# Kernel tuning notes

Hardware: AMD Instinct MI355X
Metric: run time of the kernel (lower is better)

Reference implementation:

```python
import jax, jax.numpy as jnp
import numpy as np
from jax import lax

D_MODEL = 1024
BATCH = 4
SEQ = 4096
DECAY = 0.9
INPUT_SCALE = 0.1


def setup_inputs() -> dict:
    key = jax.random.key(0)
    k1, k2, k3 = jax.random.split(key, 3)
    scale_in = 1.0 / np.sqrt(D_MODEL)
    return {
        "x": jax.random.normal(k1, (BATCH, SEQ, D_MODEL), dtype=jnp.float32),
        "W_in": jax.random.normal(k2, (D_MODEL, 2 * D_MODEL), dtype=jnp.float32) * scale_in,
        "b_in": jnp.zeros((2 * D_MODEL,), dtype=jnp.float32),
        "W_out": jax.random.normal(k3, (D_MODEL, D_MODEL), dtype=jnp.float32) * scale_in,
        "b_out": jnp.zeros((D_MODEL,), dtype=jnp.float32),
    }


def reference(x, W_in, b_in, W_out, b_out):
    # x: [B, S, D]
    x_proj = jnp.einsum("bsd,de->bse", x, W_in) + b_in  # [B, S, 2D]
    x_gate, x_hidden = jnp.split(x_proj, 2, axis=-1)
    x_gated = jax.nn.sigmoid(x_gate) * jax.nn.silu(x_hidden)  # [B, S, D]

    # gated EMA scan: h_t = 0.9*h_{t-1} + 0.1*g_t, h_0 = 0
    def step(h, g_t):
        h = DECAY * h + INPUT_SCALE * g_t
        return h, h

    g_tm = jnp.swapaxes(x_gated, 0, 1)  # [S, B, D] time-major
    h0 = jnp.zeros((x.shape[0], x.shape[2]), dtype=x.dtype)
    _, hs = lax.scan(step, h0, g_tm)  # [S, B, D]
    hidden_seq = jnp.swapaxes(hs, 0, 1)  # [B, S, D]

    out = jnp.einsum("bsd,de->bse", hidden_seq, W_out) + b_out
    return out
```

## Files before the change

### kernel.cpp

```cpp
#include <hip/hip_runtime.h>
#include <hip/hip_bf16.h>

#define B_   4
#define S_   4096
#define D_   1024
#define M_   (B_ * S_)
#define K_   1024
#define BK   64
#define NT   (K_ / BK)

typedef __attribute__((ext_vector_type(4))) float f32x4;
typedef __attribute__((ext_vector_type(8))) short bf16x8;
typedef unsigned short ushort_t;
typedef unsigned int uint_t;

__device__ inline ushort_t f2bf(float f) {
    union { float f; unsigned u; } v; v.f = f;
    unsigned r = v.u + 0x7fffu + ((v.u >> 16) & 1u);
    return (ushort_t)(r >> 16);
}
__device__ inline float bf2f(ushort_t s) {
    union { unsigned u; float f; } v; v.u = ((unsigned)s) << 16; return v.f;
}

__global__ void convert_x_kernel(const float4* __restrict__ x, ushort_t* __restrict__ xb) {
    int i = blockIdx.x * 256 + threadIdx.x;
    float4 a = x[2 * i], b = x[2 * i + 1];
    union { ushort_t s[8]; uint4 v; } u;
    u.s[0] = f2bf(a.x); u.s[1] = f2bf(a.y); u.s[2] = f2bf(a.z); u.s[3] = f2bf(a.w);
    u.s[4] = f2bf(b.x); u.s[5] = f2bf(b.y); u.s[6] = f2bf(b.z); u.s[7] = f2bf(b.w);
    ((uint4*)xb)[i] = u.v;
}

__global__ void transpose_win_kernel(const float* __restrict__ W, ushort_t* __restrict__ WT) {
    __shared__ float tile[32][33];
    int tx = threadIdx.x, ty = threadIdx.y;
    int n0 = blockIdx.x * 32, k0 = blockIdx.y * 32;
    int ci = (n0 >> 1) + (tx & 15) + ((tx & 16) ? 1024 : 0);
    tile[ty][tx] = W[(long)(k0 + ty) * 2048 + ci];
    __syncthreads();
    WT[(long)(n0 + ty) * 1024 + k0 + tx] = f2bf(tile[tx][ty]);
}

__global__ void transpose_wo_kernel(const float* __restrict__ W, ushort_t* __restrict__ WT) {
    __shared__ float tile[32][33];
    int tx = threadIdx.x, ty = threadIdx.y;
    int n0 = blockIdx.x * 32, k0 = blockIdx.y * 32;
    tile[ty][tx] = W[(long)(k0 + ty) * 1024 + n0 + tx];
    __syncthreads();
    WT[(long)(n0 + ty) * 1024 + k0 + tx] = f2bf(tile[tx][ty]);
}

__device__ inline void stage_half(const char* gtile, char* ldst, int soff0, int soff1, int w) {
    __builtin_amdgcn_global_load_lds((const __attribute__((address_space(1))) void*)(gtile + soff0),
                                     (__attribute__((address_space(3))) void*)(ldst + w * 2048), 16, 0, 0);
    __builtin_amdgcn_global_load_lds((const __attribute__((address_space(1))) void*)(gtile + soff1),
                                     (__attribute__((address_space(3))) void*)(ldst + w * 2048 + 1024), 16, 0, 0);
}

template<int NBN, int GATE>
__global__ __launch_bounds__(512, 2) void gemm8_kernel(
    const ushort_t* __restrict__ A, const ushort_t* __restrict__ Bm,
    const float* __restrict__ bias, void* __restrict__ outp)
{
    extern __shared__ char smem[];
    const int tid = threadIdx.x;
    const int l = tid & 63, w = tid >> 6;
    const int wm = w >> 2, wn = w & 3;
    const int lrow = l & 15, kgrp = l >> 4;

    const int nwg = gridDim.x;
    const int cpx = nwg >> 3;
    const int bid = blockIdx.x;
    const int wg = (bid & 7) * cpx + (bid >> 3);
    const long m0 = (long)(wg / NBN) * 256;
    const long n0 = (long)(wg % NBN) * 256;

    const char* gA = (const char*)A + m0 * 2048;
    const char* gB = (const char*)Bm + n0 * 2048;

    const int lsw = (((l & 7) ^ (l >> 3)) << 4);
    const int soff0 = ((w * 2 + 0) * 8 + (l >> 3)) * 2048 + lsw;
    const int soff1 = ((w * 2 + 1) * 8 + (l >> 3)) * 2048 + lsw;

    const int arow = (wm * 128 + lrow) * 128;
    const int brow = (wn * 64 + lrow) * 128;
    const int sw0 = (((0 * 4 + kgrp) ^ (l & 7)) << 4);
    const int sw1 = (((1 * 4 + kgrp) ^ (l & 7)) << 4);

    f32x4 acc[8][4];
#pragma unroll
    for (int i = 0; i < 8; ++i)
#pragma unroll
        for (int j = 0; j < 4; ++j) acc[i][j] = f32x4{0.f, 0.f, 0.f, 0.f};

    stage_half(gA, smem, soff0, soff1, w);
    stage_half(gB, smem + 32768, soff0, soff1, w);
    stage_half(gA + 262144, smem + 16384, soff0, soff1, w);
    stage_half(gB + 262144, smem + 32768 + 16384, soff0, soff1, w);
    stage_half(gA + 128, smem + 65536, soff0, soff1, w);
    stage_half(gB + 128, smem + 65536 + 32768, soff0, soff1, w);
    asm volatile("s_waitcnt vmcnt(4)" ::: "memory");
    __builtin_amdgcn_s_barrier();

    for (int t = 0; t < NT; ++t) {
        const int cur = t & 1, nxt = cur ^ 1;
        char* cA = smem + cur * 65536;
        char* cB = cA + 32768;
        char* oA = smem + nxt * 65536;
        char* oB = oA + 32768;
        bf16x8 af[4][2], bf[2][2], af2[4][2], bf2[2][2];

#pragma unroll
        for (int fm = 0; fm < 4; ++fm) {
            af[fm][0] = *(const bf16x8*)(cA + arow + fm * 2048 + sw0);
            af[fm][1] = *(const bf16x8*)(cA + arow + fm * 2048 + sw1);
        }
#pragma unroll
        for (int fn = 0; fn < 2; ++fn) {
            bf[fn][0] = *(const bf16x8*)(cB + brow + fn * 2048 + sw0);
            bf[fn][1] = *(const bf16x8*)(cB + brow + fn * 2048 + sw1);
        }
        if (t + 1 < NT) stage_half(gA + 262144 + (t + 1) * 128, oA + 16384, soff0, soff1, w);
        __builtin_amdgcn_s_barrier();
        __builtin_amdgcn_s_setprio(1);
#pragma unroll
        for (int fm = 0; fm < 4; ++fm)
#pragma unroll
            for (int fn = 0; fn < 2; ++fn) {
                acc[fm][fn] = __builtin_amdgcn_mfma_f32_16x16x32_bf16(af[fm][0], bf[fn][0], acc[fm][fn], 0, 0, 0);
                acc[fm][fn] = __builtin_amdgcn_mfma_f32_16x16x32_bf16(af[fm][1], bf[fn][1], acc[fm][fn], 0, 0, 0);
            }
        __builtin_amdgcn_s_setprio(0);
        __builtin_amdgcn_s_barrier();

#pragma unroll
        for (int fn = 0; fn < 2; ++fn) {
            bf2[fn][0] = *(const bf16x8*)(cB + brow + (fn + 2) * 2048 + sw0);
            bf2[fn][1] = *(const bf16x8*)(cB + brow + (fn + 2) * 2048 + sw1);
        }
        if (t + 1 < NT) stage_half(gB + 262144 + (t + 1) * 128, oB + 16384, soff0, soff1, w);
        __builtin_amdgcn_s_barrier();
        __builtin_amdgcn_s_setprio(1);
#pragma unroll
        for (int fm = 0; fm < 4; ++fm)
#pragma unroll
            for (int fn = 0; fn < 2; ++fn) {
                acc[fm][fn + 2] = __builtin_amdgcn_mfma_f32_16x16x32_bf16(af[fm][0], bf2[fn][0], acc[fm][fn + 2], 0, 0, 0);
                acc[fm][fn + 2] = __builtin_amdgcn_mfma_f32_16x16x32_bf16(af[fm][1], bf2[fn][1], acc[fm][fn + 2], 0, 0, 0);
            }
        __builtin_amdgcn_s_setprio(0);
        __builtin_amdgcn_s_barrier();

#pragma unroll
        for (int fm = 0; fm < 4; ++fm) {
            af2[fm][0] = *(const bf16x8*)(cA + arow + (fm + 4) * 2048 + sw0);
            af2[fm][1] = *(const bf16x8*)(cA + arow + (fm + 4) * 2048 + sw1);
        }
        if (t + 2 < NT) stage_half(gB + (t + 2) * 128, cB, soff0, soff1, w);
        __builtin_amdgcn_s_barrier();
        __builtin_amdgcn_s_setprio(1);
#pragma unroll
        for (int fm = 0; fm < 4; ++fm)
#pragma unroll
            for (int fn = 0; fn < 2; ++fn) {
                acc[fm + 4][fn] = __builtin_amdgcn_mfma_f32_16x16x32_bf16(af2[fm][0], bf[fn][0], acc[fm + 4][fn], 0, 0, 0);
                acc[fm + 4][fn] = __builtin_amdgcn_mfma_f32_16x16x32_bf16(af2[fm][1], bf[fn][1], acc[fm + 4][fn], 0, 0, 0);
            }
        __builtin_amdgcn_s_setprio(0);
        __builtin_amdgcn_s_barrier();

        if (t + 2 < NT) stage_half(gA + (t + 2) * 128, cA, soff0, soff1, w);
        __builtin_amdgcn_s_barrier();
        __builtin_amdgcn_s_setprio(1);
#pragma unroll
        for (int fm = 0; fm < 4; ++fm)
#pragma unroll
            for (int fn = 0; fn < 2; ++fn) {
                acc[fm + 4][fn + 2] = __builtin_amdgcn_mfma_f32_16x16x32_bf16(af2[fm][0], bf2[fn][0], acc[fm + 4][fn + 2], 0, 0, 0);
                acc[fm + 4][fn + 2] = __builtin_amdgcn_mfma_f32_16x16x32_bf16(af2[fm][1], bf2[fn][1], acc[fm + 4][fn + 2], 0, 0, 0);
            }
        __builtin_amdgcn_s_setprio(0);
        if (t < NT - 2)       asm volatile("s_waitcnt vmcnt(4)" ::: "memory");
        else if (t == NT - 2) asm volatile("s_waitcnt vmcnt(0)" ::: "memory");
        __builtin_amdgcn_s_barrier();
    }

    const long row0 = m0 + wm * 128 + kgrp * 4;
    if (GATE) {
        ushort_t* g = (ushort_t*)outp;
#pragma unroll
        for (int fm = 0; fm < 8; ++fm) {
#pragma unroll
            for (int fp = 0; fp < 2; ++fp) {
                int c = (int)(n0 >> 1) + wn * 32 + fp * 16 + lrow;
                float bg = bias[c], bh = bias[1024 + c];
#pragma unroll
                for (int r = 0; r < 4; ++r) {
                    long rr = row0 + fm * 16 + r;
                    float gate = acc[fm][fp * 2][r] + bg;
                    float hid  = acc[fm][fp * 2 + 1][r] + bh;
                    float sg = 1.0f / (1.0f + expf(-gate));
                    float sh = 1.0f / (1.0f + expf(-hid));
                    g[rr * 1024 + c] = f2bf(sg * hid * sh);
                }
            }
        }
    } else {
        float* o = (float*)outp;
#pragma unroll
        for (int fm = 0; fm < 8; ++fm)
#pragma unroll
            for (int fn = 0; fn < 4; ++fn) {
                int c = (int)n0 + wn * 64 + fn * 16 + lrow;
                float bo = bias[c];
#pragma unroll
                for (int r = 0; r < 4; ++r) {
                    long rr = row0 + fm * 16 + r;
                    o[rr * 1024 + c] = acc[fm][fn][r] + bo;
                }
            }
    }
}

__global__ void scan_kernel(const ushort_t* __restrict__ g, ushort_t* __restrict__ h) {
    int idx = blockIdx.x * 256 + threadIdx.x;
    int b = idx >> 9, d = (idx & 511) * 2;
    int chunk = blockIdx.y;
    const ushort_t* gb = g + (long)b * S_ * 1024 + d;
    ushort_t* hb = h + (long)b * S_ * 1024 + d;
    float h0 = 0.f, h1 = 0.f;
    int t0 = chunk * 256;
    int tw = t0 - 96; if (tw < 0) tw = 0;
    for (int t = tw; t < t0; ++t) {
        uint_t v = *(const uint_t*)(gb + (long)t * 1024);
        h0 = 0.9f * h0 + 0.1f * bf2f((ushort_t)(v & 0xffffu));
        h1 = 0.9f * h1 + 0.1f * bf2f((ushort_t)(v >> 16));
    }
    for (int t = t0; t < t0 + 256; ++t) {
        uint_t v = *(const uint_t*)(gb + (long)t * 1024);
        h0 = 0.9f * h0 + 0.1f * bf2f((ushort_t)(v & 0xffffu));
        h1 = 0.9f * h1 + 0.1f * bf2f((ushort_t)(v >> 16));
        *(uint_t*)(hb + (long)t * 1024) = (((uint_t)f2bf(h1)) << 16) | (uint_t)f2bf(h0);
    }
}

extern "C" void kernel_launch(void* const* d_in, const int* in_sizes, int n_in,
                              void* d_out, int out_size, void* d_ws, size_t ws_size,
                              hipStream_t stream) {
    const float* x     = (const float*)d_in[0];
    const float* W_in  = (const float*)d_in[1];
    const float* b_in  = (const float*)d_in[2];
    const float* W_out = (const float*)d_in[3];
    const float* b_out = (const float*)d_in[4];
    float* outp = (float*)d_out;

    char* ws = (char*)d_ws;
    ushort_t* xb   = (ushort_t*)ws;
    ushort_t* winT = (ushort_t*)(ws + 33554432);
    ushort_t* woT  = (ushort_t*)(ws + 33554432 + 4194304);
    ushort_t* gbuf = (ushort_t*)(ws + 33554432 + 6291456);

    hipFuncSetAttribute((const void*)&gemm8_kernel<8, 1>, hipFuncAttributeMaxDynamicSharedMemorySize, 131072);
    hipFuncSetAttribute((const void*)&gemm8_kernel<4, 0>, hipFuncAttributeMaxDynamicSharedMemorySize, 131072);

    convert_x_kernel<<<8192, 256, 0, stream>>>((const float4*)x, xb);
    transpose_win_kernel<<<dim3(64, 32), dim3(32, 32), 0, stream>>>(W_in, winT);
    transpose_wo_kernel<<<dim3(32, 32), dim3(32, 32), 0, stream>>>(W_out, woT);
    gemm8_kernel<8, 1><<<512, 512, 131072, stream>>>(xb, winT, b_in, (void*)gbuf);
    scan_kernel<<<dim3(8, 16), 256, 0, stream>>>(gbuf, xb);
    gemm8_kernel<4, 0><<<256, 512, 131072, stream>>>(xb, woT, b_out, (void*)outp);
}
```

Measured before the change: 208.6 us.

## Restructure GEMM main loop into k-half register double buffering with fewer barriers

Replaces the four-phase per-tile schedule (quarter-tile LDS reads, staggered half-tile global staging, four barriers) with a two-phase loop. Each phase issues all 32 MFMAs for one k-half, while the LDS fragments for the other k-half are loaded ahead into registers. Whole next-next tiles are staged after a single barrier, with explicit lgkmcnt/vmcnt waits and sched_barrier fences. This aims to cut barrier count and overlap LDS reads with MFMA work. In exchange it raises VGPR pressure and waits for vmcnt(0) every iteration, which may expose global load latency.

```diff
diff --git a/kernel.cpp b/kernel.cpp
--- a/kernel.cpp
+++ b/kernel.cpp
@@ -13,6 +13,9 @@
 typedef __attribute__((ext_vector_type(8))) short bf16x8;
 typedef unsigned short ushort_t;
 typedef unsigned int uint_t;
+
+#define SCHEDB __builtin_amdgcn_sched_barrier(0)
+#define MFMA16(a, b, c) __builtin_amdgcn_mfma_f32_16x16x32_bf16(a, b, c, 0, 0, 0)
 
 __device__ inline ushort_t f2bf(float f) {
     union { float f; unsigned u; } v; v.f = f;
@@ -94,97 +97,76 @@
 #pragma unroll
         for (int j = 0; j < 4; ++j) acc[i][j] = f32x4{0.f, 0.f, 0.f, 0.f};
 
-    stage_half(gA, smem, soff0, soff1, w);
-    stage_half(gB, smem + 32768, soff0, soff1, w);
-    stage_half(gA + 262144, smem + 16384, soff0, soff1, w);
-    stage_half(gB + 262144, smem + 32768 + 16384, soff0, soff1, w);
-    stage_half(gA + 128, smem + 65536, soff0, soff1, w);
-    stage_half(gB + 128, smem + 65536 + 32768, soff0, soff1, w);
-    asm volatile("s_waitcnt vmcnt(4)" ::: "memory");
+#define STAGE_TILE(t, buf)                                                    \
+    do {                                                                      \
+        const char* sa_ = gA + (t) * 128;                                     \
+        const char* sb_ = gB + (t) * 128;                                     \
+        stage_half(sa_,          (buf),          soff0, soff1, w);            \
+        stage_half(sa_ + 262144, (buf) + 16384,  soff0, soff1, w);            \
+        stage_half(sb_,          (buf) + 32768,  soff0, soff1, w);            \
+        stage_half(sb_ + 262144, (buf) + 49152,  soff0, soff1, w);            \
+    } while (0)
+
+    STAGE_TILE(0, smem);
+    STAGE_TILE(1, smem + 65536);
+    asm volatile("s_waitcnt vmcnt(8)" ::: "memory");
     __builtin_amdgcn_s_barrier();
+    SCHEDB;
+
+    bf16x8 a0[8], b0[4], a1[8], b1[4];
+#pragma unroll
+    for (int fm = 0; fm < 8; ++fm) a0[fm] = *(const bf16x8*)(smem + arow + fm * 2048 + sw0);
+#pragma unroll
+    for (int fn = 0; fn < 4; ++fn) b0[fn] = *(const bf16x8*)(smem + 32768 + brow + fn * 2048 + sw0);
 
     for (int t = 0; t < NT; ++t) {
-        const int cur = t & 1, nxt = cur ^ 1;
-        char* cA = smem + cur * 65536;
+        char* cA = smem + ((t & 1) << 16);
         char* cB = cA + 32768;
-        char* oA = smem + nxt * 65536;
-        char* oB = oA + 32768;
-        bf16x8 af[4][2], bf[2][2], af2[4][2], bf2[2][2];
-
-#pragma unroll
-        for (int fm = 0; fm < 4; ++fm) {
-            af[fm][0] = *(const bf16x8*)(cA + arow + fm * 2048 + sw0);
-            af[fm][1] = *(const bf16x8*)(cA + arow + fm * 2048 + sw1);
+        char* nA = smem + (((t + 1) & 1) << 16);
+        char* nB = nA + 32768;
+
+#pragma unroll
+        for (int fm = 0; fm < 8; ++fm) a1[fm] = *(const bf16x8*)(cA + arow + fm * 2048 + sw1);
+#pragma unroll
+        for (int fn = 0; fn < 4; ++fn) b1[fn] = *(const bf16x8*)(cB + brow + fn * 2048 + sw1);
+
+        asm volatile("s_waitcnt lgkmcnt(12)" ::: "memory");
+        SCHEDB;
+
+        __builtin_amdgcn_s_setprio(1);
+#pragma unroll
+        for (int fm = 0; fm < 8; ++fm)
+#pragma unroll
+            for (int fn = 0; fn < 4; ++fn)
+                acc[fm][fn] = MFMA16(a0[fm], b0[fn], acc[fm][fn]);
+        __builtin_amdgcn_s_setprio(0);
+        SCHEDB;
+
+        asm volatile("s_waitcnt lgkmcnt(0)" ::: "memory");
+        asm volatile("s_waitcnt vmcnt(0)" ::: "memory");
+        __builtin_amdgcn_s_barrier();
+        SCHEDB;
+
+        if (t + 2 < NT) STAGE_TILE(t + 2, cA);
+
+        if (t + 1 < NT) {
+#pragma unroll
+            for (int fm = 0; fm < 8; ++fm) a0[fm] = *(const bf16x8*)(nA + arow + fm * 2048 + sw0);
+#pragma unroll
+            for (int fn = 0; fn < 4; ++fn) b0[fn] = *(const bf16x8*)(nB + brow + fn * 2048 + sw0);
         }
-#pragma unroll
-        for (int fn = 0; fn < 2; ++fn) {
-            bf[fn][0] = *(const bf16x8*)(cB + brow + fn * 2048 + sw0);
-            bf[fn][1] = *(const bf16x8*)(cB + brow + fn * 2048 + sw1);
-        }
-        if (t + 1 < NT) stage_half(gA + 262144 + (t + 1) * 128, oA + 16384, soff0, soff1, w);
-        __builtin_amdgcn_s_barrier();
+        SCHEDB;
+
         __builtin_amdgcn_s_setprio(1);
 #pragma unroll
-        for (int fm = 0; fm < 4; ++fm)
-#pragma unroll
-            for (int fn = 0; fn < 2; ++fn) {
-                acc[fm][fn] = __builtin_amdgcn_mfma_f32_16x16x32_bf16(af[fm][0], bf[fn][0], acc[fm][fn], 0, 0, 0);
-                acc[fm][fn] = __builtin_amdgcn_mfma_f32_16x16x32_bf16(af[fm][1], bf[fn][1], acc[fm][fn], 0, 0, 0);
-            }
+        for (int fm = 0; fm < 8; ++fm)
+#pragma unroll
+            for (int fn = 0; fn < 4; ++fn)
+                acc[fm][fn] = MFMA16(a1[fm], b1[fn], acc[fm][fn]);
         __builtin_amdgcn_s_setprio(0);
-        __builtin_amdgcn_s_barrier();
-
-#pragma unroll
-        for (int fn = 0; fn < 2; ++fn) {
-            bf2[fn][0] = *(const bf16x8*)(cB + brow + (fn + 2) * 2048 + sw0);
-            bf2[fn][1] = *(const bf16x8*)(cB + brow + (fn + 2) * 2048 + sw1);
-        }
-        if (t + 1 < NT) stage_half(gB + 262144 + (t + 1) * 128, oB + 16384, soff0, soff1, w);
-        __builtin_amdgcn_s_barrier();
-        __builtin_amdgcn_s_setprio(1);
-#pragma unroll
-        for (int fm = 0; fm < 4; ++fm)
-#pragma unroll
-            for (int fn = 0; fn < 2; ++fn) {
-                acc[fm][fn + 2] = __builtin_amdgcn_mfma_f32_16x16x32_bf16(af[fm][0], bf2[fn][0], acc[fm][fn + 2], 0, 0, 0);
-                acc[fm][fn + 2] = __builtin_amdgcn_mfma_f32_16x16x32_bf16(af[fm][1], bf2[fn][1], acc[fm][fn + 2], 0, 0, 0);
-            }
-        __builtin_amdgcn_s_setprio(0);
-        __builtin_amdgcn_s_barrier();
-
-#pragma unroll
-        for (int fm = 0; fm < 4; ++fm) {
-            af2[fm][0] = *(const bf16x8*)(cA + arow + (fm + 4) * 2048 + sw0);
-            af2[fm][1] = *(const bf16x8*)(cA + arow + (fm + 4) * 2048 + sw1);
-        }
-        if (t + 2 < NT) stage_half(gB + (t + 2) * 128, cB, soff0, soff1, w);
-        __builtin_amdgcn_s_barrier();
-        __builtin_amdgcn_s_setprio(1);
-#pragma unroll
-        for (int fm = 0; fm < 4; ++fm)
-#pragma unroll
-            for (int fn = 0; fn < 2; ++fn) {
-                acc[fm + 4][fn] = __builtin_amdgcn_mfma_f32_16x16x32_bf16(af2[fm][0], bf[fn][0], acc[fm + 4][fn], 0, 0, 0);
-                acc[fm + 4][fn] = __builtin_amdgcn_mfma_f32_16x16x32_bf16(af2[fm][1], bf[fn][1], acc[fm + 4][fn], 0, 0, 0);
-            }
-        __builtin_amdgcn_s_setprio(0);
-        __builtin_amdgcn_s_barrier();
-
-        if (t + 2 < NT) stage_half(gA + (t + 2) * 128, cA, soff0, soff1, w);
-        __builtin_amdgcn_s_barrier();
-        __builtin_amdgcn_s_setprio(1);
-#pragma unroll
-        for (int fm = 0; fm < 4; ++fm)
-#pragma unroll
-            for (int fn = 0; fn < 2; ++fn) {
-                acc[fm + 4][fn + 2] = __builtin_amdgcn_mfma_f32_16x16x32_bf16(af2[fm][0], bf2[fn][0], acc[fm + 4][fn + 2], 0, 0, 0);
-                acc[fm + 4][fn + 2] = __builtin_amdgcn_mfma_f32_16x16x32_bf16(af2[fm][1], bf2[fn][1], acc[fm + 4][fn + 2], 0, 0, 0);
-            }
-        __builtin_amdgcn_s_setprio(0);
-        if (t < NT - 2)       asm volatile("s_waitcnt vmcnt(4)" ::: "memory");
-        else if (t == NT - 2) asm volatile("s_waitcnt vmcnt(0)" ::: "memory");
-        __builtin_amdgcn_s_barrier();
-    }
+        SCHEDB;
+    }
+#undef STAGE_TILE
 
     const long row0 = m0 + wm * 128 + kgrp * 4;
     if (GATE) {
```

Measured after the change: 205.7 us. Within noise of the previous version (-1.4%).

## Restructure GEMM main loop with register prefetch and finer waits; split scan chunks

Applied to the files above, without the earlier changes.

Reorders the GEMM inner loop so the next tile's A/B fragments are loaded from LDS during the last MFMA phase, replaces some barriers with explicit vmcnt/lgkmcnt waits and sched_barrier fences, and reorders global->LDS staging. Launch bounds change to one block per CU minimum occupancy hint, giving the compiler more registers. The scan kernel uses 128-step chunks (doubling grid) with unrolled loops for more parallelism, at the cost of relatively more warmup recomputation. The approximate 96-step warmup already existed.

```diff
diff --git a/kernel.cpp b/kernel.cpp
--- a/kernel.cpp
+++ b/kernel.cpp
@@ -13,6 +13,9 @@
 typedef __attribute__((ext_vector_type(8))) short bf16x8;
 typedef unsigned short ushort_t;
 typedef unsigned int uint_t;
+
+#define SCHEDB __builtin_amdgcn_sched_barrier(0)
+#define MFMA16(a, b, c) __builtin_amdgcn_mfma_f32_16x16x32_bf16(a, b, c, 0, 0, 0)
 
 __device__ inline ushort_t f2bf(float f) {
     union { float f; unsigned u; } v; v.f = f;
@@ -59,7 +62,7 @@
 }
 
 template<int NBN, int GATE>
-__global__ __launch_bounds__(512, 2) void gemm8_kernel(
+__global__ __launch_bounds__(512, 1) void gemm8_kernel(
     const ushort_t* __restrict__ A, const ushort_t* __restrict__ Bm,
     const float* __restrict__ bias, void* __restrict__ outp)
 {
@@ -69,9 +72,7 @@
     const int wm = w >> 2, wn = w & 3;
     const int lrow = l & 15, kgrp = l >> 4;
 
-    const int nwg = gridDim.x;
-    const int cpx = nwg >> 3;
-    const int bid = blockIdx.x;
+    const int nwg = gridDim.x, cpx = nwg >> 3, bid = blockIdx.x;
     const int wg = (bid & 7) * cpx + (bid >> 3);
     const long m0 = (long)(wg / NBN) * 256;
     const long n0 = (long)(wg % NBN) * 256;
@@ -85,8 +86,8 @@
 
     const int arow = (wm * 128 + lrow) * 128;
     const int brow = (wn * 64 + lrow) * 128;
-    const int sw0 = (((0 * 4 + kgrp) ^ (l & 7)) << 4);
-    const int sw1 = (((1 * 4 + kgrp) ^ (l & 7)) << 4);
+    const int sw0 = ((kgrp ^ (l & 7)) << 4);
+    const int sw1 = (((4 + kgrp) ^ (l & 7)) << 4);
 
     f32x4 acc[8][4];
 #pragma unroll
@@ -94,95 +95,122 @@
 #pragma unroll
         for (int j = 0; j < 4; ++j) acc[i][j] = f32x4{0.f, 0.f, 0.f, 0.f};
 
-    stage_half(gA, smem, soff0, soff1, w);
-    stage_half(gB, smem + 32768, soff0, soff1, w);
-    stage_half(gA + 262144, smem + 16384, soff0, soff1, w);
-    stage_half(gB + 262144, smem + 32768 + 16384, soff0, soff1, w);
-    stage_half(gA + 128, smem + 65536, soff0, soff1, w);
-    stage_half(gB + 128, smem + 65536 + 32768, soff0, soff1, w);
-    asm volatile("s_waitcnt vmcnt(4)" ::: "memory");
+    bf16x8 af[4][2], bf[2][2], af2[4][2], bf2[2][2];
+
+    char* s1 = smem + 65536;
+    stage_half(gA,              smem,          soff0, soff1, w);
+    stage_half(gA + 262144,     smem + 16384,  soff0, soff1, w);
+    stage_half(gB,              smem + 32768,  soff0, soff1, w);
+    stage_half(gB + 262144,     smem + 49152,  soff0, soff1, w);
+    stage_half(gA + 128,        s1,            soff0, soff1, w);
+    stage_half(gA + 262144 + 128, s1 + 16384,  soff0, soff1, w);
+    stage_half(gB + 128,        s1 + 32768,    soff0, soff1, w);
+    stage_half(gB + 262144 + 128, s1 + 49152,  soff0, soff1, w);
+    asm volatile("s_waitcnt vmcnt(8)" ::: "memory");
     __builtin_amdgcn_s_barrier();
+#pragma unroll
+    for (int fm = 0; fm < 4; ++fm) {
+        af[fm][0] = *(const bf16x8*)(smem + arow + fm * 2048 + sw0);
+        af[fm][1] = *(const bf16x8*)(smem + arow + fm * 2048 + sw1);
+    }
+#pragma unroll
+    for (int fn = 0; fn < 2; ++fn) {
+        bf[fn][0] = *(const bf16x8*)(smem + 32768 + brow + fn * 2048 + sw0);
+        bf[fn][1] = *(const bf16x8*)(smem + 32768 + brow + fn * 2048 + sw1);
+    }
+    SCHEDB;
 
     for (int t = 0; t < NT; ++t) {
-        const int cur = t & 1, nxt = cur ^ 1;
-        char* cA = smem + cur * 65536;
-        char* cB = cA + 32768;
-        char* oA = smem + nxt * 65536;
-        char* oB = oA + 32768;
-        bf16x8 af[4][2], bf[2][2], af2[4][2], bf2[2][2];
+        char* cur = smem + ((t & 1) << 16);
+        char* nxt = smem + (((t + 1) & 1) << 16);
+
+#pragma unroll
+        for (int fn = 0; fn < 2; ++fn) {
+            bf2[fn][0] = *(const bf16x8*)(cur + 32768 + brow + (fn + 2) * 2048 + sw0);
+            bf2[fn][1] = *(const bf16x8*)(cur + 32768 + brow + (fn + 2) * 2048 + sw1);
+        }
+        SCHEDB;
+        asm volatile("s_waitcnt vmcnt(4)" ::: "memory");
+        asm volatile("s_waitcnt lgkmcnt(4)" ::: "memory");
+        SCHEDB;
+        __builtin_amdgcn_s_setprio(1);
+#pragma unroll
+        for (int fm = 0; fm < 4; ++fm)
+#pragma unroll
+            for (int fn = 0; fn < 2; ++fn) {
+                acc[fm][fn] = MFMA16(af[fm][0], bf[fn][0], acc[fm][fn]);
+                acc[fm][fn] = MFMA16(af[fm][1], bf[fn][1], acc[fm][fn]);
+            }
+        __builtin_amdgcn_s_setprio(0);
+        SCHEDB;
+        __builtin_amdgcn_s_barrier();
 
 #pragma unroll
         for (int fm = 0; fm < 4; ++fm) {
-            af[fm][0] = *(const bf16x8*)(cA + arow + fm * 2048 + sw0);
-            af[fm][1] = *(const bf16x8*)(cA + arow + fm * 2048 + sw1);
-        }
-#pragma unroll
-        for (int fn = 0; fn < 2; ++fn) {
-            bf[fn][0] = *(const bf16x8*)(cB + brow + fn * 2048 + sw0);
-            bf[fn][1] = *(const bf16x8*)(cB + brow + fn * 2048 + sw1);
-        }
-        if (t + 1 < NT) stage_half(gA + 262144 + (t + 1) * 128, oA + 16384, soff0, soff1, w);
+            af2[fm][0] = *(const bf16x8*)(cur + arow + (fm + 4) * 2048 + sw0);
+            af2[fm][1] = *(const bf16x8*)(cur + arow + (fm + 4) * 2048 + sw1);
+        }
+        if (t + 2 < NT) stage_half(gA + (t + 2) * 128, cur, soff0, soff1, w);
+        SCHEDB;
+        asm volatile("s_waitcnt lgkmcnt(8)" ::: "memory");
+        SCHEDB;
+        __builtin_amdgcn_s_setprio(1);
+#pragma unroll
+        for (int fm = 0; fm < 4; ++fm)
+#pragma unroll
+            for (int fn = 0; fn < 2; ++fn) {
+                acc[fm][fn + 2] = MFMA16(af[fm][0], bf2[fn][0], acc[fm][fn + 2]);
+                acc[fm][fn + 2] = MFMA16(af[fm][1], bf2[fn][1], acc[fm][fn + 2]);
+            }
+        __builtin_amdgcn_s_setprio(0);
+        SCHEDB;
         __builtin_amdgcn_s_barrier();
+
+        if (t + 2 < NT) stage_half(gB + (t + 2) * 128, cur + 32768, soff0, soff1, w);
+        SCHEDB;
+        if (t < NT - 2) asm volatile("s_waitcnt vmcnt(6)" ::: "memory");
+        else            asm volatile("s_waitcnt vmcnt(0)" ::: "memory");
+        asm volatile("s_waitcnt lgkmcnt(0)" ::: "memory");
+        SCHEDB;
         __builtin_amdgcn_s_setprio(1);
 #pragma unroll
         for (int fm = 0; fm < 4; ++fm)
 #pragma unroll
             for (int fn = 0; fn < 2; ++fn) {
-                acc[fm][fn] = __builtin_amdgcn_mfma_f32_16x16x32_bf16(af[fm][0], bf[fn][0], acc[fm][fn], 0, 0, 0);
-                acc[fm][fn] = __builtin_amdgcn_mfma_f32_16x16x32_bf16(af[fm][1], bf[fn][1], acc[fm][fn], 0, 0, 0);
+                acc[fm + 4][fn] = MFMA16(af2[fm][0], bf[fn][0], acc[fm + 4][fn]);
+                acc[fm + 4][fn] = MFMA16(af2[fm][1], bf[fn][1], acc[fm + 4][fn]);
             }
         __builtin_amdgcn_s_setprio(0);
+        SCHEDB;
         __builtin_amdgcn_s_barrier();
 
-#pragma unroll
-        for (int fn = 0; fn < 2; ++fn) {
-            bf2[fn][0] = *(const bf16x8*)(cB + brow + (fn + 2) * 2048 + sw0);
-            bf2[fn][1] = *(const bf16x8*)(cB + brow + (fn + 2) * 2048 + sw1);
-        }
-        if (t + 1 < NT) stage_half(gB + 262144 + (t + 1) * 128, oB + 16384, soff0, soff1, w);
-        __builtin_amdgcn_s_barrier();
+        if (t + 1 < NT) {
+#pragma unroll
+            for (int fm = 0; fm < 4; ++fm) {
+                af[fm][0] = *(const bf16x8*)(nxt + arow + fm * 2048 + sw0);
+                af[fm][1] = *(const bf16x8*)(nxt + arow + fm * 2048 + sw1);
+            }
+#pragma unroll
+            for (int fn = 0; fn < 2; ++fn) {
+                bf[fn][0] = *(const bf16x8*)(nxt + 32768 + brow + fn * 2048 + sw0);
+                bf[fn][1] = *(const bf16x8*)(nxt + 32768 + brow + fn * 2048 + sw1);
+            }
+        }
+        if (t + 2 < NT) {
+            stage_half(gB + 262144 + (t + 2) * 128, cur + 49152, soff0, soff1, w);
+            stage_half(gA + 262144 + (t + 2) * 128, cur + 16384, soff0, soff1, w);
+        }
+        SCHEDB;
         __builtin_amdgcn_s_setprio(1);
 #pragma unroll
         for (int fm = 0; fm < 4; ++fm)
 #pragma unroll
             for (int fn = 0; fn < 2; ++fn) {
-                acc[fm][fn + 2] = __builtin_amdgcn_mfma_f32_16x16x32_bf16(af[fm][0], bf2[fn][0], acc[fm][fn + 2], 0, 0, 0);
-                acc[fm][fn + 2] = __builtin_amdgcn_mfma_f32_16x16x32_bf16(af[fm][1], bf2[fn][1], acc[fm][fn + 2], 0, 0, 0);
+                acc[fm + 4][fn + 2] = MFMA16(af2[fm][0], bf2[fn][0], acc[fm + 4][fn + 2]);
+                acc[fm + 4][fn + 2] = MFMA16(af2[fm][1], bf2[fn][1], acc[fm + 4][fn + 2]);
             }
         __builtin_amdgcn_s_setprio(0);
-        __builtin_amdgcn_s_barrier();
-
-#pragma unroll
-        for (int fm = 0; fm < 4; ++fm) {
-            af2[fm][0] = *(const bf16x8*)(cA + arow + (fm + 4) * 2048 + sw0);
-            af2[fm][1] = *(const bf16x8*)(cA + arow + (fm + 4) * 2048 + sw1);
-        }
-        if (t + 2 < NT) stage_half(gB + (t + 2) * 128, cB, soff0, soff1, w);
-        __builtin_amdgcn_s_barrier();
-        __builtin_amdgcn_s_setprio(1);
-#pragma unroll
-        for (int fm = 0; fm < 4; ++fm)
-#pragma unroll
-            for (int fn = 0; fn < 2; ++fn) {
-                acc[fm + 4][fn] = __builtin_amdgcn_mfma_f32_16x16x32_bf16(af2[fm][0], bf[fn][0], acc[fm + 4][fn], 0, 0, 0);
-                acc[fm + 4][fn] = __builtin_amdgcn_mfma_f32_16x16x32_bf16(af2[fm][1], bf[fn][1], acc[fm + 4][fn], 0, 0, 0);
-            }
-        __builtin_amdgcn_s_setprio(0);
-        __builtin_amdgcn_s_barrier();
-
-        if (t + 2 < NT) stage_half(gA + (t + 2) * 128, cA, soff0, soff1, w);
-        __builtin_amdgcn_s_barrier();
-        __builtin_amdgcn_s_setprio(1);
-#pragma unroll
-        for (int fm = 0; fm < 4; ++fm)
-#pragma unroll
-            for (int fn = 0; fn < 2; ++fn) {
-                acc[fm + 4][fn + 2] = __builtin_amdgcn_mfma_f32_16x16x32_bf16(af2[fm][0], bf2[fn][0], acc[fm + 4][fn + 2], 0, 0, 0);
-                acc[fm + 4][fn + 2] = __builtin_amdgcn_mfma_f32_16x16x32_bf16(af2[fm][1], bf2[fn][1], acc[fm + 4][fn + 2], 0, 0, 0);
-            }
-        __builtin_amdgcn_s_setprio(0);
-        if (t < NT - 2)       asm volatile("s_waitcnt vmcnt(4)" ::: "memory");
-        else if (t == NT - 2) asm volatile("s_waitcnt vmcnt(0)" ::: "memory");
+        SCHEDB;
         __builtin_amdgcn_s_barrier();
     }
 
@@ -230,14 +258,16 @@
     const ushort_t* gb = g + (long)b * S_ * 1024 + d;
     ushort_t* hb = h + (long)b * S_ * 1024 + d;
     float h0 = 0.f, h1 = 0.f;
-    int t0 = chunk * 256;
+    int t0 = chunk * 128;
     int tw = t0 - 96; if (tw < 0) tw = 0;
+#pragma unroll 4
     for (int t = tw; t < t0; ++t) {
         uint_t v = *(const uint_t*)(gb + (long)t * 1024);
         h0 = 0.9f * h0 + 0.1f * bf2f((ushort_t)(v & 0xffffu));
         h1 = 0.9f * h1 + 0.1f * bf2f((ushort_t)(v >> 16));
     }
-    for (int t = t0; t < t0 + 256; ++t) {
+#pragma unroll 4
+    for (int t = t0; t < t0 + 128; ++t) {
         uint_t v = *(const uint_t*)(gb + (long)t * 1024);
         h0 = 0.9f * h0 + 0.1f * bf2f((ushort_t)(v & 0xffffu));
         h1 = 0.9f * h1 + 0.1f * bf2f((ushort_t)(v >> 16));
@@ -268,6 +298,6 @@
     transpose_win_kernel<<<dim3(64, 32), dim3(32, 32), 0, stream>>>(W_in, winT);
     transpose_wo_kernel<<<dim3(32, 32), dim3(32, 32), 0, stream>>>(W_out, woT);
     gemm8_kernel<8, 1><<<512, 512, 131072, stream>>>(xb, winT, b_in, (void*)gbuf);
-    scan_kernel<<<dim3(8, 16), 256, 0, stream>>>(gbuf, xb);
+    scan_kernel<<<dim3(8, 32), 256, 0, stream>>>(gbuf, xb);
     gemm8_kernel<4, 0><<<256, 512, 131072, stream>>>(xb, woT, b_out, (void*)outp);
 }
```

Result: faster. 175.7 us (-15.8%).
